# Optimization experiments

Hardware: AMD Instinct MI355X
Metric: run time of the kernel (lower is better)

Reference implementation:

```python
import jax, jax.numpy as jnp
import numpy as np
import math

N = 512            # batch
D = 512            # in_features (embedding dim)
C = 50000          # out_features (num classes)
S = 30.0           # scale
M = 0.5            # margin
COS_M = math.cos(M)
SIN_M = math.sin(M)
TH = math.cos(math.pi - M)
MM = math.sin(math.pi - M) * M


def _l2norm(x, eps=1e-12):
    # torch F.normalize: x / max(||x||_2, eps) along dim=1
    n = jnp.sqrt(jnp.sum(x * x, axis=1, keepdims=True))
    return x / jnp.maximum(n, eps)


def setup_inputs() -> dict:
    key = jax.random.key(0)
    k1, k2, k3 = jax.random.split(key, 3)
    logits = jax.random.normal(k1, (N, D), dtype=jnp.float32)
    labels = jax.random.randint(k2, (N,), 0, C, dtype=jnp.int64)
    # xavier_uniform over (C, D): bound = sqrt(6/(C+D))
    bound = math.sqrt(6.0 / (C + D))
    weight = jax.random.uniform(k3, (C, D), dtype=jnp.float32, minval=-bound, maxval=bound)
    return {"logits": logits, "labels": labels, "weight": weight}


def reference(logits, labels, weight):
    x = _l2norm(logits)                      # [N, D]
    w = _l2norm(weight)                      # [C, D]
    cosine = jnp.einsum('nd,cd->nc', x, w)   # [N, C]
    sine = jnp.sqrt(jnp.clip(1.0 + 1e-7 - cosine * cosine, 0.0, 1.0))
    phi = cosine * COS_M - sine * SIN_M
    # easy_margin=False branch
    phi = jnp.where(cosine > TH, phi, cosine - MM)
    onehot = jax.nn.one_hot(labels, C, dtype=cosine.dtype)  # [N, C]
    output = (onehot * phi + (1.0 - onehot) * cosine) * S
    # CrossEntropyLoss(reduction='none') then .mean()
    logp = jax.nn.log_softmax(output, axis=1)
    loss_per = -jnp.take_along_axis(logp, labels[:, None], axis=1)[:, 0]
    loss = jnp.mean(loss_per)
    return output, loss
```

## Files before the change

### kernel.cpp

```cpp
#include <hip/hip_runtime.h>
#include <stdint.h>

#define N_B   512
#define D_K   512
#define C_N   50000
#define C_PAD 50048
#define BM    128
#define BN    128
#define BK    32
#define NCB   391

#define S_SCALE 30.0f
#define COS_Mc  0.87758256189037276f
#define SIN_Mc  0.47942553860420301f
#define TH_Cc  (-0.87758256189037276f)
#define MM_Cc   0.23971276930210156f
#define NEG_BIG (-3.0e38f)

typedef __attribute__((ext_vector_type(8))) __bf16 bf16x8;
typedef __attribute__((ext_vector_type(4))) float  f32x4;

__device__ __forceinline__ unsigned short f2bf(float f) {
    union { float f; unsigned u; } v; v.f = f;
    unsigned r = v.u + 0x7FFFu + ((v.u >> 16) & 1u);
    return (unsigned short)(r >> 16);
}

__device__ __forceinline__ void gl2lds16(const void* g, void* l) {
    __builtin_amdgcn_global_load_lds(
        (__attribute__((address_space(1))) unsigned int*)(g),
        (__attribute__((address_space(3))) unsigned int*)(l),
        16, 0, 0);
}

__global__ __launch_bounds__(256) void prep_kernel(
        const float* __restrict__ src, unsigned short* __restrict__ dstb,
        float* __restrict__ inv, int nvalid, int ntotal)
{
    int wave = threadIdx.x >> 6, lane = threadIdx.x & 63;
    int row = blockIdx.x * 4 + wave;
    if (row >= ntotal) return;
    unsigned short* dst = dstb + (size_t)row * D_K + lane * 8;
    if (row < nvalid) {
        const float4* s4 = (const float4*)(src + (size_t)row * D_K) + lane * 2;
        float4 a = s4[0], b = s4[1];
        float ss = a.x*a.x + a.y*a.y + a.z*a.z + a.w*a.w
                 + b.x*b.x + b.y*b.y + b.z*b.z + b.w*b.w;
        #pragma unroll
        for (int off = 32; off >= 1; off >>= 1) ss += __shfl_xor(ss, off, 64);
        if (lane == 0) inv[row] = 1.0f / fmaxf(sqrtf(ss), 1e-12f);
        uint4 o;
        o.x = (unsigned)f2bf(a.x) | ((unsigned)f2bf(a.y) << 16);
        o.y = (unsigned)f2bf(a.z) | ((unsigned)f2bf(a.w) << 16);
        o.z = (unsigned)f2bf(b.x) | ((unsigned)f2bf(b.y) << 16);
        o.w = (unsigned)f2bf(b.z) | ((unsigned)f2bf(b.w) << 16);
        *(uint4*)dst = o;
    } else {
        *(uint4*)dst = make_uint4(0u, 0u, 0u, 0u);
        if (lane == 0) inv[row] = 0.0f;
    }
}

__global__ __launch_bounds__(256) void gemm_margin_kernel(
        const unsigned short* __restrict__ xb, const unsigned short* __restrict__ wb,
        const float* __restrict__ invx, const float* __restrict__ invw,
        const int* __restrict__ labels, float* __restrict__ out,
        float* __restrict__ m_part, float* __restrict__ s_part)
{
    const int cb = blockIdx.x, rb = blockIdx.y;
    const int m0 = rb * BM, c0 = cb * BN;
    const int tid = threadIdx.x;
    const int lane = tid & 63, wave = tid >> 6;
    const int wm = wave >> 1, wn = wave & 1;
    const int l15 = lane & 15, q = lane >> 4;

    __shared__ __align__(16) unsigned short As[BM * BK];
    __shared__ __align__(16) unsigned short Bs[BN * BK];
    __shared__ float s_invx[BM];
    __shared__ float s_invw[BN];
    __shared__ int   s_lab[BM];
    __shared__ float sm[2][BM];
    __shared__ float ssm[2][BM];

    if (tid < BM) {
        s_invx[tid] = invx[m0 + tid];
        s_lab[tid]  = labels[m0 + tid];
        s_invw[tid] = invw[c0 + tid];
    }

    f32x4 zero4 = {0.f, 0.f, 0.f, 0.f};
    f32x4 acc[4][4];
    #pragma unroll
    for (int i = 0; i < 4; i++)
        #pragma unroll
        for (int j = 0; j < 4; j++) acc[i][j] = zero4;

    const int srow   = tid >> 2;
    const int pchunk = tid & 3;
    const int lch0 = pchunk ^ ((srow >> 1) & 3);
    const int lch1 = pchunk ^ (((srow + 64) >> 1) & 3);

    const unsigned short* gA0 = xb + (size_t)(m0 + srow)      * D_K + lch0 * 8;
    const unsigned short* gA1 = xb + (size_t)(m0 + srow + 64) * D_K + lch1 * 8;
    const unsigned short* gB0 = wb + (size_t)(c0 + srow)      * D_K + lch0 * 8;
    const unsigned short* gB1 = wb + (size_t)(c0 + srow + 64) * D_K + lch1 * 8;

    unsigned short* lA0 = As + srow * BK + pchunk * 8;
    unsigned short* lA1 = As + (srow + 64) * BK + pchunk * 8;
    unsigned short* lB0 = Bs + srow * BK + pchunk * 8;
    unsigned short* lB1 = Bs + (srow + 64) * BK + pchunk * 8;

    int aoff[4], boff[4];
    #pragma unroll
    for (int i = 0; i < 4; i++) {
        int Ra = wm * 64 + i * 16 + l15;
        aoff[i] = Ra * BK + (q ^ ((Ra >> 1) & 3)) * 8;
        int Rb = wn * 64 + i * 16 + l15;
        boff[i] = Rb * BK + (q ^ ((Rb >> 1) & 3)) * 8;
    }

    for (int k0 = 0; k0 < D_K; k0 += BK) {
        gl2lds16(gA0 + k0, lA0);
        gl2lds16(gA1 + k0, lA1);
        gl2lds16(gB0 + k0, lB0);
        gl2lds16(gB1 + k0, lB1);
        __syncthreads();

        bf16x8 af[4], bf[4];
        #pragma unroll
        for (int i = 0; i < 4; i++) af[i] = *(const bf16x8*)(As + aoff[i]);
        #pragma unroll
        for (int i = 0; i < 4; i++) bf[i] = *(const bf16x8*)(Bs + boff[i]);
        #pragma unroll
        for (int mi = 0; mi < 4; mi++)
            #pragma unroll
            for (int ni = 0; ni < 4; ni++)
                acc[mi][ni] = __builtin_amdgcn_mfma_f32_16x16x32_bf16(
                                  af[mi], bf[ni], acc[mi][ni], 0, 0, 0);
        __syncthreads();
    }

    float rm[16], rs[16];
    #pragma unroll
    for (int mi = 0; mi < 4; mi++) {
        #pragma unroll
        for (int r = 0; r < 4; r++) {
            int lrow = wm * 64 + mi * 16 + q * 4 + r;
            int grow = m0 + lrow;
            float ivx = s_invx[lrow];
            int lab = s_lab[lrow];
            float tv[4]; bool ok[4];
            float vmax = NEG_BIG;
            #pragma unroll
            for (int ni = 0; ni < 4; ni++) {
                int lcol = wn * 64 + ni * 16 + l15;
                int gcol = c0 + lcol;
                float cosv = acc[mi][ni][r] * ivx * s_invw[lcol];
                float o;
                if (gcol == lab) {
                    float s2 = 1.0f + 1e-7f - cosv * cosv;
                    s2 = fminf(fmaxf(s2, 0.0f), 1.0f);
                    float phi = cosv * COS_Mc - sqrtf(s2) * SIN_Mc;
                    if (!(cosv > TH_Cc)) phi = cosv - MM_Cc;
                    o = S_SCALE * phi;
                } else {
                    o = S_SCALE * cosv;
                }
                ok[ni] = (gcol < C_N);
                tv[ni] = o;
                if (ok[ni]) {
                    out[(size_t)grow * C_N + gcol] = o;
                    vmax = fmaxf(vmax, o);
                }
            }
            float vs = 0.f;
            #pragma unroll
            for (int ni = 0; ni < 4; ni++)
                if (ok[ni]) vs += __expf(tv[ni] - vmax);
            rm[mi * 4 + r] = vmax;
            rs[mi * 4 + r] = vs;
        }
    }
    #pragma unroll
    for (int off = 1; off < 16; off <<= 1) {
        #pragma unroll
        for (int i = 0; i < 16; i++) {
            float om = __shfl_xor(rm[i], off, 64);
            float os = __shfl_xor(rs[i], off, 64);
            float M = fmaxf(rm[i], om);
            rs[i] = rs[i] * __expf(rm[i] - M) + os * __expf(om - M);
            rm[i] = M;
        }
    }
    if (l15 == 0) {
        #pragma unroll
        for (int i = 0; i < 16; i++) {
            int mi = i >> 2, r = i & 3;
            int lrow = wm * 64 + mi * 16 + q * 4 + r;
            sm[wn][lrow]  = rm[i];
            ssm[wn][lrow] = rs[i];
        }
    }
    __syncthreads();
    if (tid < BM) {
        float m1 = sm[0][tid], s1 = ssm[0][tid];
        float m2 = sm[1][tid], s2 = ssm[1][tid];
        float M = fmaxf(m1, m2);
        float S = s1 * __expf(m1 - M) + s2 * __expf(m2 - M);
        m_part[(size_t)(m0 + tid) * NCB + cb] = M;
        s_part[(size_t)(m0 + tid) * NCB + cb] = S;
    }
}

__global__ void rowreduce_kernel(
        const float* __restrict__ m_part, const float* __restrict__ s_part,
        const float* __restrict__ out, const int* __restrict__ labels,
        float* __restrict__ lossp)
{
    int row = blockIdx.x;
    int lane = threadIdx.x;
    float m = NEG_BIG, s = 0.f;
    for (int j = lane; j < NCB; j += 64) {
        float m2 = m_part[(size_t)row * NCB + j];
        float s2 = s_part[(size_t)row * NCB + j];
        float M = fmaxf(m, m2);
        s = s * __expf(m - M) + s2 * __expf(m2 - M);
        m = M;
    }
    #pragma unroll
    for (int off = 1; off < 64; off <<= 1) {
        float om = __shfl_xor(m, off, 64);
        float os = __shfl_xor(s, off, 64);
        float M = fmaxf(m, om);
        s = s * __expf(m - M) + os * __expf(om - M);
        m = M;
    }
    if (lane == 0) {
        float logZ = m + logf(s);
        int lab = labels[row];
        lossp[row] = logZ - out[(size_t)row * C_N + lab];
    }
}

__global__ void loss_kernel(const float* __restrict__ lossp, float* __restrict__ loss_out) {
    int t = threadIdx.x;
    float v = lossp[t] + lossp[t + 256];
    #pragma unroll
    for (int off = 32; off >= 1; off >>= 1) v += __shfl_xor(v, off, 64);
    __shared__ float part[4];
    if ((t & 63) == 0) part[t >> 6] = v;
    __syncthreads();
    if (t == 0) loss_out[0] = (part[0] + part[1] + part[2] + part[3]) * (1.0f / 512.0f);
}

extern "C" void kernel_launch(void* const* d_in, const int* in_sizes, int n_in,
                              void* d_out, int out_size, void* d_ws, size_t ws_size,
                              hipStream_t stream)
{
    const float* x      = (const float*)d_in[0];
    const int*   labels = (const int*)d_in[1];
    const float* w      = (const float*)d_in[2];
    float* out = (float*)d_out;
    float* loss_out = out + (size_t)N_B * C_N;

    char* ws = (char*)d_ws;
    size_t off = 0;
    unsigned short* xb = (unsigned short*)(ws + off); off += (size_t)N_B * D_K * 2;
    unsigned short* wb = (unsigned short*)(ws + off); off += (size_t)C_PAD * D_K * 2;
    float* invx   = (float*)(ws + off); off += (size_t)N_B * 4;
    float* invw   = (float*)(ws + off); off += (size_t)C_PAD * 4;
    float* m_part = (float*)(ws + off); off += (size_t)N_B * NCB * 4;
    float* s_part = (float*)(ws + off); off += (size_t)N_B * NCB * 4;
    float* lossp  = (float*)(ws + off); off += (size_t)N_B * 4;

    prep_kernel<<<N_B / 4, 256, 0, stream>>>(x, xb, invx, N_B, N_B);
    prep_kernel<<<C_PAD / 4, 256, 0, stream>>>(w, wb, invw, C_N, C_PAD);
    dim3 grid(NCB, N_B / BM);
    gemm_margin_kernel<<<grid, 256, 0, stream>>>(xb, wb, invx, invw, labels,
                                                 out, m_part, s_part);
    rowreduce_kernel<<<N_B, 64, 0, stream>>>(m_part, s_part, out, labels, lossp);
    loss_kernel<<<1, 256, 0, stream>>>(lossp, loss_out);
}
```

Baseline: 268.1 us.

## Fuse weight normalization into GEMM, keep full-K weight tile in LDS, fixed-shift softmax

Drops the separate weight prep pass: each GEMM block loads a 64-column fp32 weight slice, converts it to bf16 into a swizzled full-K LDS tile, and computes the column norms in place. A-operands are read straight from global memory with no K-loop barriers, and each block covers 256 rows, with two blocks sharing each weight slice. The online max is replaced by a fixed shift of 30, which relies on outputs being bounded by the scale. The row reduction becomes a plain sum over a transposed partial buffer. This removes the bf16 weight round trip and the max bookkeeping, but the weights are read from fp32 twice (once per row half) and the 64KB LDS tile limits occupancy.

```diff
diff --git a/kernel.cpp b/kernel.cpp
--- a/kernel.cpp
+++ b/kernel.cpp
@@ -4,18 +4,16 @@
 #define N_B   512
 #define D_K   512
 #define C_N   50000
-#define C_PAD 50048
-#define BM    128
-#define BN    128
-#define BK    32
-#define NCB   391
+#define BN    64
+#define NCB   782
+#define C_PAD (NCB * BN)
 
 #define S_SCALE 30.0f
 #define COS_Mc  0.87758256189037276f
 #define SIN_Mc  0.47942553860420301f
 #define TH_Cc  (-0.87758256189037276f)
 #define MM_Cc   0.23971276930210156f
-#define NEG_BIG (-3.0e38f)
+#define SHIFT   30.0f
 
 typedef __attribute__((ext_vector_type(8))) __bf16 bf16x8;
 typedef __attribute__((ext_vector_type(4))) float  f32x4;
@@ -26,68 +24,82 @@
     return (unsigned short)(r >> 16);
 }
 
-__device__ __forceinline__ void gl2lds16(const void* g, void* l) {
-    __builtin_amdgcn_global_load_lds(
-        (__attribute__((address_space(1))) unsigned int*)(g),
-        (__attribute__((address_space(3))) unsigned int*)(l),
-        16, 0, 0);
-}
-
-__global__ __launch_bounds__(256) void prep_kernel(
+__global__ __launch_bounds__(256) void prep_x_kernel(
         const float* __restrict__ src, unsigned short* __restrict__ dstb,
-        float* __restrict__ inv, int nvalid, int ntotal)
+        float* __restrict__ inv)
 {
     int wave = threadIdx.x >> 6, lane = threadIdx.x & 63;
     int row = blockIdx.x * 4 + wave;
-    if (row >= ntotal) return;
-    unsigned short* dst = dstb + (size_t)row * D_K + lane * 8;
-    if (row < nvalid) {
-        const float4* s4 = (const float4*)(src + (size_t)row * D_K) + lane * 2;
-        float4 a = s4[0], b = s4[1];
-        float ss = a.x*a.x + a.y*a.y + a.z*a.z + a.w*a.w
-                 + b.x*b.x + b.y*b.y + b.z*b.z + b.w*b.w;
+    const float4* s4 = (const float4*)(src + (size_t)row * D_K) + lane * 2;
+    float4 a = s4[0], b = s4[1];
+    float ss = a.x*a.x + a.y*a.y + a.z*a.z + a.w*a.w
+             + b.x*b.x + b.y*b.y + b.z*b.z + b.w*b.w;
+    #pragma unroll
+    for (int off = 32; off >= 1; off >>= 1) ss += __shfl_xor(ss, off, 64);
+    if (lane == 0) inv[row] = 1.0f / fmaxf(sqrtf(ss), 1e-12f);
+    uint4 o;
+    o.x = (unsigned)f2bf(a.x) | ((unsigned)f2bf(a.y) << 16);
+    o.y = (unsigned)f2bf(a.z) | ((unsigned)f2bf(a.w) << 16);
+    o.z = (unsigned)f2bf(b.x) | ((unsigned)f2bf(b.y) << 16);
+    o.w = (unsigned)f2bf(b.z) | ((unsigned)f2bf(b.w) << 16);
+    *(uint4*)(dstb + (size_t)row * D_K + lane * 8) = o;
+}
+
+__global__ __launch_bounds__(256, 2) void gemm2_kernel(
+        const unsigned short* __restrict__ xb, const float* __restrict__ w,
+        const float* __restrict__ invx, const int* __restrict__ labels,
+        float* __restrict__ out, float* __restrict__ s_part)
+{
+    const int half = blockIdx.x;
+    const int cb   = blockIdx.y;
+    const int c0   = cb * BN;
+    const int rbase = half * 256;
+    const int tid  = threadIdx.x;
+    const int lane = tid & 63, wave = tid >> 6;
+    const int l15  = lane & 15, q = lane >> 4;
+
+    __shared__ __align__(16) unsigned short Ws[BN * D_K];
+    __shared__ float s_invw[BN];
+    __shared__ float s_invx[256];
+    __shared__ int   s_lab[256];
+
+    s_invx[tid] = invx[rbase + tid];
+    s_lab[tid]  = labels[rbase + tid];
+
+    #pragma unroll 4
+    for (int i = 0; i < 32; i++) {
+        int flat = i * 1024 + tid * 4;
+        int col = flat >> 9, k = flat & 511;
+        int gcol = c0 + col;
+        float4 v = make_float4(0.f, 0.f, 0.f, 0.f);
+        if (gcol < C_N) v = *(const float4*)(w + (size_t)gcol * D_K + k);
+        uint2 p;
+        p.x = (unsigned)f2bf(v.x) | ((unsigned)f2bf(v.y) << 16);
+        p.y = (unsigned)f2bf(v.z) | ((unsigned)f2bf(v.w) << 16);
+        int idx = col * D_K + (((k >> 3) ^ (col & 7)) << 3) + (k & 7);
+        *(uint2*)(Ws + idx) = p;
+    }
+    __syncthreads();
+
+    for (int p = 0; p < 16; p++) {
+        int c = wave * 16 + p;
+        int addr = c * D_K + (((lane ^ (c & 7)) & 63) << 3);
+        uint4 u = *(const uint4*)(Ws + addr);
+        float ss = 0.f;
+        #pragma unroll
+        for (int j = 0; j < 4; j++) {
+            unsigned word = (&u.x)[j];
+            float a = __uint_as_float(word << 16);
+            float b = __uint_as_float(word & 0xffff0000u);
+            ss += a * a + b * b;
+        }
         #pragma unroll
         for (int off = 32; off >= 1; off >>= 1) ss += __shfl_xor(ss, off, 64);
-        if (lane == 0) inv[row] = 1.0f / fmaxf(sqrtf(ss), 1e-12f);
-        uint4 o;
-        o.x = (unsigned)f2bf(a.x) | ((unsigned)f2bf(a.y) << 16);
-        o.y = (unsigned)f2bf(a.z) | ((unsigned)f2bf(a.w) << 16);
-        o.z = (unsigned)f2bf(b.x) | ((unsigned)f2bf(b.y) << 16);
-        o.w = (unsigned)f2bf(b.z) | ((unsigned)f2bf(b.w) << 16);
-        *(uint4*)dst = o;
-    } else {
-        *(uint4*)dst = make_uint4(0u, 0u, 0u, 0u);
-        if (lane == 0) inv[row] = 0.0f;
-    }
-}
-
-__global__ __launch_bounds__(256) void gemm_margin_kernel(
-        const unsigned short* __restrict__ xb, const unsigned short* __restrict__ wb,
-        const float* __restrict__ invx, const float* __restrict__ invw,
-        const int* __restrict__ labels, float* __restrict__ out,
-        float* __restrict__ m_part, float* __restrict__ s_part)
-{
-    const int cb = blockIdx.x, rb = blockIdx.y;
-    const int m0 = rb * BM, c0 = cb * BN;
-    const int tid = threadIdx.x;
-    const int lane = tid & 63, wave = tid >> 6;
-    const int wm = wave >> 1, wn = wave & 1;
-    const int l15 = lane & 15, q = lane >> 4;
-
-    __shared__ __align__(16) unsigned short As[BM * BK];
-    __shared__ __align__(16) unsigned short Bs[BN * BK];
-    __shared__ float s_invx[BM];
-    __shared__ float s_invw[BN];
-    __shared__ int   s_lab[BM];
-    __shared__ float sm[2][BM];
-    __shared__ float ssm[2][BM];
-
-    if (tid < BM) {
-        s_invx[tid] = invx[m0 + tid];
-        s_lab[tid]  = labels[m0 + tid];
-        s_invw[tid] = invw[c0 + tid];
-    }
-
+        if (lane == 0) s_invw[c] = 1.0f / fmaxf(sqrtf(ss), 1e-12f);
+    }
+    __syncthreads();
+
+    const int r0 = rbase + wave * 64;
     f32x4 zero4 = {0.f, 0.f, 0.f, 0.f};
     f32x4 acc[4][4];
     #pragma unroll
@@ -95,150 +107,81 @@
         #pragma unroll
         for (int j = 0; j < 4; j++) acc[i][j] = zero4;
 
-    const int srow   = tid >> 2;
-    const int pchunk = tid & 3;
-    const int lch0 = pchunk ^ ((srow >> 1) & 3);
-    const int lch1 = pchunk ^ (((srow + 64) >> 1) & 3);
-
-    const unsigned short* gA0 = xb + (size_t)(m0 + srow)      * D_K + lch0 * 8;
-    const unsigned short* gA1 = xb + (size_t)(m0 + srow + 64) * D_K + lch1 * 8;
-    const unsigned short* gB0 = wb + (size_t)(c0 + srow)      * D_K + lch0 * 8;
-    const unsigned short* gB1 = wb + (size_t)(c0 + srow + 64) * D_K + lch1 * 8;
-
-    unsigned short* lA0 = As + srow * BK + pchunk * 8;
-    unsigned short* lA1 = As + (srow + 64) * BK + pchunk * 8;
-    unsigned short* lB0 = Bs + srow * BK + pchunk * 8;
-    unsigned short* lB1 = Bs + (srow + 64) * BK + pchunk * 8;
-
-    int aoff[4], boff[4];
-    #pragma unroll
-    for (int i = 0; i < 4; i++) {
-        int Ra = wm * 64 + i * 16 + l15;
-        aoff[i] = Ra * BK + (q ^ ((Ra >> 1) & 3)) * 8;
-        int Rb = wn * 64 + i * 16 + l15;
-        boff[i] = Rb * BK + (q ^ ((Rb >> 1) & 3)) * 8;
-    }
-
-    for (int k0 = 0; k0 < D_K; k0 += BK) {
-        gl2lds16(gA0 + k0, lA0);
-        gl2lds16(gA1 + k0, lA1);
-        gl2lds16(gB0 + k0, lB0);
-        gl2lds16(gB1 + k0, lB1);
-        __syncthreads();
-
-        bf16x8 af[4], bf[4];
-        #pragma unroll
-        for (int i = 0; i < 4; i++) af[i] = *(const bf16x8*)(As + aoff[i]);
-        #pragma unroll
-        for (int i = 0; i < 4; i++) bf[i] = *(const bf16x8*)(Bs + boff[i]);
+    const unsigned short* Abase = xb + (size_t)(r0 + l15) * D_K + q * 8;
+
+    #pragma unroll
+    for (int ks = 0; ks < 16; ks++) {
+        bf16x8 af[4], bfr[4];
+        #pragma unroll
+        for (int mi = 0; mi < 4; mi++)
+            af[mi] = *(const bf16x8*)(Abase + mi * 16 * D_K + ks * 32);
+        #pragma unroll
+        for (int ni = 0; ni < 4; ni++) {
+            int nc = ni * 16 + l15;
+            int ch = (ks * 4 + q) ^ (nc & 7);
+            bfr[ni] = *(const bf16x8*)(Ws + nc * D_K + ch * 8);
+        }
         #pragma unroll
         for (int mi = 0; mi < 4; mi++)
             #pragma unroll
             for (int ni = 0; ni < 4; ni++)
                 acc[mi][ni] = __builtin_amdgcn_mfma_f32_16x16x32_bf16(
-                                  af[mi], bf[ni], acc[mi][ni], 0, 0, 0);
-        __syncthreads();
-    }
-
-    float rm[16], rs[16];
+                                  af[mi], bfr[ni], acc[mi][ni], 0, 0, 0);
+    }
+
     #pragma unroll
     for (int mi = 0; mi < 4; mi++) {
         #pragma unroll
         for (int r = 0; r < 4; r++) {
-            int lrow = wm * 64 + mi * 16 + q * 4 + r;
-            int grow = m0 + lrow;
+            int lrow = wave * 64 + mi * 16 + q * 4 + r;
+            int grow = rbase + lrow;
             float ivx = s_invx[lrow];
             int lab = s_lab[lrow];
-            float tv[4]; bool ok[4];
-            float vmax = NEG_BIG;
+            float es = 0.f;
             #pragma unroll
             for (int ni = 0; ni < 4; ni++) {
-                int lcol = wn * 64 + ni * 16 + l15;
-                int gcol = c0 + lcol;
-                float cosv = acc[mi][ni][r] * ivx * s_invw[lcol];
-                float o;
+                int gcol = c0 + ni * 16 + l15;
+                float cosv = acc[mi][ni][r] * ivx * s_invw[ni * 16 + l15];
+                float o = S_SCALE * cosv;
                 if (gcol == lab) {
-                    float s2 = 1.0f + 1e-7f - cosv * cosv;
-                    s2 = fminf(fmaxf(s2, 0.0f), 1.0f);
+                    float s2 = fminf(fmaxf(1.0f + 1e-7f - cosv * cosv, 0.f), 1.f);
                     float phi = cosv * COS_Mc - sqrtf(s2) * SIN_Mc;
                     if (!(cosv > TH_Cc)) phi = cosv - MM_Cc;
                     o = S_SCALE * phi;
-                } else {
-                    o = S_SCALE * cosv;
                 }
-                ok[ni] = (gcol < C_N);
-                tv[ni] = o;
-                if (ok[ni]) {
+                if (gcol < C_N) {
                     out[(size_t)grow * C_N + gcol] = o;
-                    vmax = fmaxf(vmax, o);
+                    es += __expf(o - SHIFT);
                 }
             }
-            float vs = 0.f;
-            #pragma unroll
-            for (int ni = 0; ni < 4; ni++)
-                if (ok[ni]) vs += __expf(tv[ni] - vmax);
-            rm[mi * 4 + r] = vmax;
-            rs[mi * 4 + r] = vs;
+            es += __shfl_xor(es, 1, 64);
+            es += __shfl_xor(es, 2, 64);
+            es += __shfl_xor(es, 4, 64);
+            es += __shfl_xor(es, 8, 64);
+            if (l15 == 0) s_part[(size_t)cb * N_B + grow] = es;
         }
     }
-    #pragma unroll
-    for (int off = 1; off < 16; off <<= 1) {
-        #pragma unroll
-        for (int i = 0; i < 16; i++) {
-            float om = __shfl_xor(rm[i], off, 64);
-            float os = __shfl_xor(rs[i], off, 64);
-            float M = fmaxf(rm[i], om);
-            rs[i] = rs[i] * __expf(rm[i] - M) + os * __expf(om - M);
-            rm[i] = M;
-        }
-    }
-    if (l15 == 0) {
-        #pragma unroll
-        for (int i = 0; i < 16; i++) {
-            int mi = i >> 2, r = i & 3;
-            int lrow = wm * 64 + mi * 16 + q * 4 + r;
-            sm[wn][lrow]  = rm[i];
-            ssm[wn][lrow] = rs[i];
-        }
-    }
-    __syncthreads();
-    if (tid < BM) {
-        float m1 = sm[0][tid], s1 = ssm[0][tid];
-        float m2 = sm[1][tid], s2 = ssm[1][tid];
-        float M = fmaxf(m1, m2);
-        float S = s1 * __expf(m1 - M) + s2 * __expf(m2 - M);
-        m_part[(size_t)(m0 + tid) * NCB + cb] = M;
-        s_part[(size_t)(m0 + tid) * NCB + cb] = S;
-    }
 }
 
 __global__ void rowreduce_kernel(
-        const float* __restrict__ m_part, const float* __restrict__ s_part,
-        const float* __restrict__ out, const int* __restrict__ labels,
-        float* __restrict__ lossp)
-{
-    int row = blockIdx.x;
-    int lane = threadIdx.x;
-    float m = NEG_BIG, s = 0.f;
-    for (int j = lane; j < NCB; j += 64) {
-        float m2 = m_part[(size_t)row * NCB + j];
-        float s2 = s_part[(size_t)row * NCB + j];
-        float M = fmaxf(m, m2);
-        s = s * __expf(m - M) + s2 * __expf(m2 - M);
-        m = M;
-    }
-    #pragma unroll
-    for (int off = 1; off < 64; off <<= 1) {
-        float om = __shfl_xor(m, off, 64);
-        float os = __shfl_xor(s, off, 64);
-        float M = fmaxf(m, om);
-        s = s * __expf(m - M) + os * __expf(om - M);
-        m = M;
-    }
-    if (lane == 0) {
-        float logZ = m + logf(s);
-        int lab = labels[row];
-        lossp[row] = logZ - out[(size_t)row * C_N + lab];
+        const float* __restrict__ s_part, const float* __restrict__ out,
+        const int* __restrict__ labels, float* __restrict__ lossp)
+{
+    int b = blockIdx.x;
+    int r = b * 64 + (threadIdx.x & 63);
+    int c = threadIdx.x >> 6;
+    float s = 0.f;
+    for (int j = c; j < NCB; j += 8) s += s_part[(size_t)j * N_B + r];
+    __shared__ float pt[8][64];
+    pt[c][threadIdx.x & 63] = s;
+    __syncthreads();
+    if (threadIdx.x < 64) {
+        int row = b * 64 + threadIdx.x;
+        float t = 0.f;
+        #pragma unroll
+        for (int cc = 0; cc < 8; cc++) t += pt[cc][threadIdx.x];
+        float logZ = SHIFT + logf(t);
+        lossp[row] = logZ - out[(size_t)row * C_N + labels[row]];
     }
 }
 
@@ -266,18 +209,12 @@
     char* ws = (char*)d_ws;
     size_t off = 0;
     unsigned short* xb = (unsigned short*)(ws + off); off += (size_t)N_B * D_K * 2;
-    unsigned short* wb = (unsigned short*)(ws + off); off += (size_t)C_PAD * D_K * 2;
     float* invx   = (float*)(ws + off); off += (size_t)N_B * 4;
-    float* invw   = (float*)(ws + off); off += (size_t)C_PAD * 4;
-    float* m_part = (float*)(ws + off); off += (size_t)N_B * NCB * 4;
-    float* s_part = (float*)(ws + off); off += (size_t)N_B * NCB * 4;
+    float* s_part = (float*)(ws + off); off += (size_t)NCB * N_B * 4;
     float* lossp  = (float*)(ws + off); off += (size_t)N_B * 4;
 
-    prep_kernel<<<N_B / 4, 256, 0, stream>>>(x, xb, invx, N_B, N_B);
-    prep_kernel<<<C_PAD / 4, 256, 0, stream>>>(w, wb, invw, C_N, C_PAD);
-    dim3 grid(NCB, N_B / BM);
-    gemm_margin_kernel<<<grid, 256, 0, stream>>>(xb, wb, invx, invw, labels,
-                                                 out, m_part, s_part);
-    rowreduce_kernel<<<N_B, 64, 0, stream>>>(m_part, s_part, out, labels, lossp);
+    prep_x_kernel<<<N_B / 4, 256, 0, stream>>>(x, xb, invx);
+    gemm2_kernel<<<dim3(2, NCB), 256, 0, stream>>>(xb, w, invx, labels, out, s_part);
+    rowreduce_kernel<<<8, 512, 0, stream>>>(s_part, out, labels, lossp);
     loss_kernel<<<1, 256, 0, stream>>>(lossp, loss_out);
 }
```

Measured after the change: 363.1 us. +35.4%, slower.
